# Kernel tuning notes

Hardware: AMD Instinct MI355X
Metric: run time of the kernel (lower is better)

The kernel has to match this reference:

```python
import jax, jax.numpy as jnp
import numpy as np

N_NODES = 500000
D = 128          # input_dim
UNITS = 128
K = 32           # neigh_max
B = 20000        # batch of target nodes
LEAKY_ALPHA = 0.2  # tf.nn.leaky_relu default


def setup_inputs() -> dict:
    key = jax.random.key(0)
    k1, k2, k3, k4, k5, k6, k7 = jax.random.split(key, 7)
    features = jax.random.normal(k1, (N_NODES, D), dtype=jnp.float32)
    node = jax.random.randint(k2, (B, 1), 0, N_NODES, dtype=jnp.int32)
    neighbours = jax.random.randint(k3, (B, K), 0, N_NODES, dtype=jnp.int32)
    # learned parameters (glorot-scale random)
    kernel = jax.random.normal(k4, (1, D, D), dtype=jnp.float32) * (1.0 / np.sqrt(D))
    kernel1 = jax.random.normal(k5, (1, D, D), dtype=jnp.float32) * (1.0 / np.sqrt(D))
    attention_weights = jax.random.normal(k6, (1, 2 * D), dtype=jnp.float32) * (1.0 / np.sqrt(2 * D))
    neigh_weights = jax.random.normal(k7, (D, UNITS), dtype=jnp.float32) * (1.0 / np.sqrt(D))
    return {
        "features": features,
        "node": node,
        "neighbours": neighbours,
        "kernel": kernel,
        "kernel1": kernel1,
        "attention_weights": attention_weights,
        "neigh_weights": neigh_weights,
    }


def reference(features, node, neighbours, kernel, kernel1, attention_weights, neigh_weights):
    # gather: node_feat [B,1,D], neigh_feat [B,K,D]
    node_feat = features[node]
    neigh_feat = features[neighbours]
    # per-node projections (kernel tiled over batch in original == shared matmul)
    node_h = jnp.einsum('bkd,de->bke', node_feat, kernel[0])    # [B,1,D]
    neigh_h = jnp.einsum('bkd,de->bke', neigh_feat, kernel1[0])  # [B,K,D]
    # concat [neigh, tiled node] -> [B,K,2D]
    tile_node = jnp.broadcast_to(node_h, neigh_h.shape)
    concat_feat = jnp.concatenate([neigh_h, tile_node], axis=2)
    # attention score: [B,K,2D] @ [2D,1] -> [B,K,1], leaky_relu (alpha=0.2)
    score = concat_feat @ attention_weights.reshape(2 * D, 1)
    score = jnp.where(score > 0, score, LEAKY_ALPHA * score)
    # softmax over neighbors (axis K)
    final_score = jax.nn.softmax(score, axis=1)                  # [B,K,1]
    # weighted aggregate: neigh_h^T @ score -> [B,D]
    attention_feat = jnp.einsum('bkd,bk->bd', neigh_h, final_score[..., 0])
    # output projection
    return attention_feat @ neigh_weights                        # [B,UNITS]
```

## Files before the change

kernel.cpp:

```cpp
#include <hip/hip_runtime.h>
#include <hip/hip_bf16.h>

#define D 128
#define K 32
#define NB 20000
#define NPB 4
#define NBLK (NB / NPB)
#define NROWS 33
#define RSTRIDE 66

typedef unsigned short u16;
typedef unsigned int   u32;

__device__ inline float blo(u32 v) { return __uint_as_float(v << 16); }
__device__ inline float bhi(u32 v) { return __uint_as_float(v & 0xffff0000u); }
__device__ inline u32 f2b_rne(float x) {
    u32 u = __float_as_uint(x);
    return (u + 0x7fffu + ((u >> 16) & 1u)) >> 16;
}
__device__ inline u32 pack2(float a, float b) { return f2b_rne(a) | (f2b_rne(b) << 16); }

__global__ __launch_bounds__(256)
void precompute_kernel(const float* __restrict__ k0, const float* __restrict__ k1,
                       const float* __restrict__ aw, const float* __restrict__ nw,
                       float* __restrict__ w12, u16* __restrict__ MTb)
{
    int t = threadIdx.x;
    if (blockIdx.x < 64) {
        int gid = blockIdx.x * 256 + t;
        int u = gid & 127, d = gid >> 7;
        float acc = 0.f;
        #pragma unroll 8
        for (int e = 0; e < D; ++e)
            acc = fmaf(k1[d * D + e], nw[e * D + u], acc);
        MTb[u * D + d] = (u16)f2b_rne(acc);
    } else {
        if (t < 128) {
            float acc = 0.f;
            #pragma unroll 8
            for (int e = 0; e < D; ++e)
                acc = fmaf(k1[t * D + e], aw[e], acc);
            w12[t] = acc;
        } else {
            int d = t - 128;
            float acc = 0.f;
            #pragma unroll 8
            for (int e = 0; e < D; ++e)
                acc = fmaf(k0[d * D + e], aw[128 + e], acc);
            w12[t] = acc;
        }
    }
}

__global__ __launch_bounds__(256)
void gat4_kernel(const float* __restrict__ features,
                 const int* __restrict__ node,
                 const int* __restrict__ neigh,
                 const float* __restrict__ w12g,
                 const u16* __restrict__ MTb,
                 float* __restrict__ out)
{
    __shared__ u32   fbuf[132 * RSTRIDE];
    __shared__ float wlds[256];
    __shared__ int   idxs[132];
    __shared__ float zb[132];
    __shared__ float alpha[128];
    __shared__ float agg[512];

    const int t  = threadIdx.x;
    const int b4 = blockIdx.x * NPB;

    wlds[t] = w12g[t];
    if (t < 132) {
        int n = t & 3, j = t >> 2;
        idxs[t] = (j < K) ? neigh[(b4 + n) * K + j] : node[b4 + n];
    }
    __syncthreads();

    const float4* f4 = (const float4*)features;
    #pragma unroll 4
    for (int c = t; c < 132 * 32; c += 256) {
        int r = c >> 5, cc = c & 31;
        float4 v = f4[(size_t)idxs[r] * 32 + cc];
        u32* dst = &fbuf[r * RSTRIDE + cc * 2];
        dst[0] = pack2(v.x, v.y);
        dst[1] = pack2(v.z, v.w);
        const float* w = &wlds[((r < 128) ? 0 : 128) + cc * 4];
        float p = v.x * w[0] + v.y * w[1] + v.z * w[2] + v.w * w[3];
        p += __shfl_xor(p, 1);
        p += __shfl_xor(p, 2);
        p += __shfl_xor(p, 4);
        p += __shfl_xor(p, 8);
        p += __shfl_xor(p, 16);
        if (cc == 0) zb[(r & 3) * 33 + (r >> 2)] = p;
    }
    __syncthreads();

    if ((t & 63) == 0) {
        int n = t >> 6;
        float cadd = zb[n * 33 + 32];
        float m = -1e30f;
        #pragma unroll
        for (int k = 0; k < K; ++k) {
            float v = zb[n * 33 + k] + cadd;
            v = v > 0.f ? v : 0.2f * v;
            alpha[n * 32 + k] = v;
            m = fmaxf(m, v);
        }
        float s = 0.f;
        #pragma unroll
        for (int k = 0; k < K; ++k) {
            float e = __expf(alpha[n * 32 + k] - m);
            alpha[n * 32 + k] = e;
            s += e;
        }
        float inv = 1.f / s;
        #pragma unroll
        for (int k = 0; k < K; ++k) alpha[n * 32 + k] *= inv;
    }
    __syncthreads();

    {
        int n = t >> 6, p = t & 63;
        float a0 = 0.f, a1 = 0.f;
        #pragma unroll
        for (int k = 0; k < K; ++k) {
            u32 v = fbuf[(4 * k + n) * RSTRIDE + p];
            float al = alpha[n * 32 + k];
            a0 = fmaf(al, blo(v), a0);
            a1 = fmaf(al, bhi(v), a1);
        }
        agg[n * 128 + 2 * p]     = a0;
        agg[n * 128 + 2 * p + 1] = a1;
    }
    __syncthreads();

    {
        int u  = t & 127;
        int nA = t >> 7;
        const uint4* mrow = (const uint4*)(MTb + u * D);
        const float* aggA = &agg[nA * 128];
        const float* aggB = &agg[(nA + 2) * 128];
        float accA0 = 0.f, accA1 = 0.f, accB0 = 0.f, accB1 = 0.f;
        #pragma unroll
        for (int q = 0; q < 16; ++q) {
            uint4 m4 = mrow[q];
            int d0 = q * 8;
            float m0 = blo(m4.x), m1 = bhi(m4.x), m2 = blo(m4.y), m3 = bhi(m4.y);
            float m4f = blo(m4.z), m5 = bhi(m4.z), m6 = blo(m4.w), m7 = bhi(m4.w);
            accA0 += aggA[d0] * m0 + aggA[d0+1] * m1 + aggA[d0+2] * m2 + aggA[d0+3] * m3;
            accA1 += aggA[d0+4] * m4f + aggA[d0+5] * m5 + aggA[d0+6] * m6 + aggA[d0+7] * m7;
            accB0 += aggB[d0] * m0 + aggB[d0+1] * m1 + aggB[d0+2] * m2 + aggB[d0+3] * m3;
            accB1 += aggB[d0+4] * m4f + aggB[d0+5] * m5 + aggB[d0+6] * m6 + aggB[d0+7] * m7;
        }
        out[(size_t)(b4 + nA) * D + u]     = accA0 + accA1;
        out[(size_t)(b4 + nA + 2) * D + u] = accB0 + accB1;
    }
}

#define RS 33
#define RSF 132
__global__ __launch_bounds__(256)
void gat_fallback_kernel(const float* __restrict__ features, const int* __restrict__ node,
                         const int* __restrict__ neigh,
                         const float* __restrict__ k0, const float* __restrict__ k1,
                         const float* __restrict__ aw, const float* __restrict__ nw,
                         float* __restrict__ out)
{
    __shared__ float4 fbuf[NROWS * RS];
    __shared__ float w1[D], w2[D], h[D];
    __shared__ int   idxs[NROWS];
    __shared__ float psum[NROWS][8];
    __shared__ float zb[NROWS], alpha[K], agg[D];

    const int b = blockIdx.x, t = threadIdx.x;

    if (t < 128) {
        float a = 0.f;
        for (int e = 0; e < D; ++e) a = fmaf(k1[t * D + e], aw[e], a);
        w1[t] = a;
    } else {
        int d = t - 128;
        float a = 0.f;
        for (int e = 0; e < D; ++e) a = fmaf(k0[d * D + e], aw[128 + e], a);
        w2[d] = a;
    }
    if (t < K)       idxs[t] = neigh[b * K + t];
    else if (t == K) idxs[K] = node[b];
    __syncthreads();

    const float4* f4 = (const float4*)features;
    for (int c = t; c < NROWS * 32; c += 256) {
        int j = c >> 5, cc = c & 31;
        fbuf[j * RS + cc] = f4[(size_t)idxs[j] * 32 + cc];
    }
    __syncthreads();

    for (int task = t; task < NROWS * 8; task += 256) {
        int j = task >> 3, sub = task & 7;
        const float* w = (j < K) ? w1 : w2;
        const float4* r = &fbuf[j * RS + sub * 4];
        int d0 = sub * 16;
        float4 a0 = r[0], a1 = r[1], a2 = r[2], a3 = r[3];
        float acc;
        acc  = a0.x * w[d0 + 0]  + a0.y * w[d0 + 1]  + a0.z * w[d0 + 2]  + a0.w * w[d0 + 3];
        acc += a1.x * w[d0 + 4]  + a1.y * w[d0 + 5]  + a1.z * w[d0 + 6]  + a1.w * w[d0 + 7];
        acc += a2.x * w[d0 + 8]  + a2.y * w[d0 + 9]  + a2.z * w[d0 + 10] + a2.w * w[d0 + 11];
        acc += a3.x * w[d0 + 12] + a3.y * w[d0 + 13] + a3.z * w[d0 + 14] + a3.w * w[d0 + 15];
        psum[j][sub] = acc;
    }
    __syncthreads();

    if (t < NROWS) {
        float s = 0.f;
        #pragma unroll
        for (int i = 0; i < 8; ++i) s += psum[t][i];
        zb[t] = s;
    }
    __syncthreads();

    if (t == 0) {
        float c = zb[K];
        float m = -1e30f;
        #pragma unroll
        for (int k = 0; k < K; ++k) {
            float v = zb[k] + c;
            v = v > 0.f ? v : 0.2f * v;
            zb[k] = v;
            m = fmaxf(m, v);
        }
        float s = 0.f;
        #pragma unroll
        for (int k = 0; k < K; ++k) { float e = __expf(zb[k] - m); alpha[k] = e; s += e; }
        float inv = 1.f / s;
        #pragma unroll
        for (int k = 0; k < K; ++k) alpha[k] *= inv;
    }
    __syncthreads();

    const float* fb = (const float*)fbuf;
    if (t < D) {
        float a = 0.f;
        #pragma unroll
        for (int k = 0; k < K; ++k)
            a = fmaf(alpha[k], fb[k * RSF + t], a);
        agg[t] = a;
    }
    __syncthreads();

    if (t < 128) {
        float acc = 0.f;
        for (int d = 0; d < D; ++d) acc = fmaf(agg[d], k1[d * D + t], acc);
        h[t] = acc;
    }
    __syncthreads();
    if (t < 128) {
        float acc = 0.f;
        for (int e = 0; e < D; ++e) acc = fmaf(h[e], nw[e * D + t], acc);
        out[(size_t)b * D + t] = acc;
    }
}

extern "C" void kernel_launch(void* const* d_in, const int* in_sizes, int n_in,
                              void* d_out, int out_size, void* d_ws, size_t ws_size,
                              hipStream_t stream) {
    const float* features = (const float*)d_in[0];
    const int*   node     = (const int*)d_in[1];
    const int*   neigh    = (const int*)d_in[2];
    const float* k0       = (const float*)d_in[3];
    const float* k1       = (const float*)d_in[4];
    const float* aw       = (const float*)d_in[5];
    const float* nw       = (const float*)d_in[6];

    const size_t need = 256 * sizeof(float) + (size_t)D * D * sizeof(u16);
    if (ws_size >= need) {
        float* w12 = (float*)d_ws;
        u16*   MTb = (u16*)(w12 + 256);
        precompute_kernel<<<65, 256, 0, stream>>>(k0, k1, aw, nw, w12, MTb);
        gat4_kernel<<<NBLK, 256, 0, stream>>>(features, node, neigh, w12, MTb,
                                              (float*)d_out);
    } else {
        gat_fallback_kernel<<<NB, 256, 0, stream>>>(features, node, neigh,
                                                    k0, k1, aw, nw, (float*)d_out);
    }
}
```

Before: 412.1 us.

## Batch all gather loads in registers and do softmax with wave shuffles

Each thread now loads its 17 neighbour and node indices straight into registers and issues all 17 float4 feature gathers before any use. This drops the index staging through LDS and its barrier and raises memory-level parallelism. The softmax moves from a single thread per node to a 32-lane shuffle reduction, and the attention weights are broadcast with __shfl, which removes the alpha LDS array and one barrier. The change costs more registers, which may lower occupancy, and drops the padded row stride, which may bring LDS bank conflicts.

```diff
diff --git a/kernel.cpp b/kernel.cpp
--- a/kernel.cpp
+++ b/kernel.cpp
@@ -7,7 +7,7 @@
 #define NPB 4
 #define NBLK (NB / NPB)
 #define NROWS 33
-#define RSTRIDE 66
+#define FSTR 64
 
 typedef unsigned short u16;
 typedef unsigned int   u32;
@@ -60,33 +60,40 @@
                  const u16* __restrict__ MTb,
                  float* __restrict__ out)
 {
-    __shared__ u32   fbuf[132 * RSTRIDE];
-    __shared__ float wlds[256];
-    __shared__ int   idxs[132];
+    __shared__ u32   fbuf[128 * FSTR];
     __shared__ float zb[132];
-    __shared__ float alpha[128];
     __shared__ float agg[512];
 
     const int t  = threadIdx.x;
     const int b4 = blockIdx.x * NPB;
-
-    wlds[t] = w12g[t];
-    if (t < 132) {
-        int n = t & 3, j = t >> 2;
-        idxs[t] = (j < K) ? neigh[(b4 + n) * K + j] : node[b4 + n];
-    }
-    __syncthreads();
+    const int cc = t & 31;
+    const int r0 = t >> 5;
+
+    const float4* w4 = (const float4*)w12g;
+    const float4 wlo = w4[cc];
+    const float4 whi = w4[32 + cc];
+
+    int idx[17];
+    #pragma unroll
+    for (int i = 0; i < 16; ++i) {
+        int r = r0 + 8 * i;
+        idx[i] = neigh[(b4 + (r & 3)) * K + (r >> 2)];
+    }
+    idx[16] = node[b4 + (r0 & 3)];
 
     const float4* f4 = (const float4*)features;
-    #pragma unroll 4
-    for (int c = t; c < 132 * 32; c += 256) {
-        int r = c >> 5, cc = c & 31;
-        float4 v = f4[(size_t)idxs[r] * 32 + cc];
-        u32* dst = &fbuf[r * RSTRIDE + cc * 2];
-        dst[0] = pack2(v.x, v.y);
-        dst[1] = pack2(v.z, v.w);
-        const float* w = &wlds[((r < 128) ? 0 : 128) + cc * 4];
-        float p = v.x * w[0] + v.y * w[1] + v.z * w[2] + v.w * w[3];
+    float4 v[17];
+    #pragma unroll
+    for (int i = 0; i < 17; ++i)
+        v[i] = f4[(size_t)idx[i] * 32 + cc];
+
+    #pragma unroll
+    for (int i = 0; i < 16; ++i) {
+        int r = r0 + 8 * i;
+        u32* dst = &fbuf[r * FSTR + cc * 2];
+        dst[0] = pack2(v[i].x, v[i].y);
+        dst[1] = pack2(v[i].z, v[i].w);
+        float p = v[i].x * wlo.x + v[i].y * wlo.y + v[i].z * wlo.z + v[i].w * wlo.w;
         p += __shfl_xor(p, 1);
         p += __shfl_xor(p, 2);
         p += __shfl_xor(p, 4);
@@ -94,44 +101,46 @@
         p += __shfl_xor(p, 16);
         if (cc == 0) zb[(r & 3) * 33 + (r >> 2)] = p;
     }
-    __syncthreads();
-
-    if ((t & 63) == 0) {
-        int n = t >> 6;
-        float cadd = zb[n * 33 + 32];
-        float m = -1e30f;
+    if (r0 < 4) {
+        float p = v[16].x * whi.x + v[16].y * whi.y + v[16].z * whi.z + v[16].w * whi.w;
+        p += __shfl_xor(p, 1);
+        p += __shfl_xor(p, 2);
+        p += __shfl_xor(p, 4);
+        p += __shfl_xor(p, 8);
+        p += __shfl_xor(p, 16);
+        if (cc == 0) zb[r0 * 33 + 32] = p;
+    }
+    __syncthreads();
+
+    {
+        const int n = t >> 6, l = t & 63, k32 = l & 31;
+        float vsc = zb[n * 33 + k32] + zb[n * 33 + 32];
+        vsc = vsc > 0.f ? vsc : 0.2f * vsc;
+        float m = vsc;
+        m = fmaxf(m, __shfl_xor(m, 1));
+        m = fmaxf(m, __shfl_xor(m, 2));
+        m = fmaxf(m, __shfl_xor(m, 4));
+        m = fmaxf(m, __shfl_xor(m, 8));
+        m = fmaxf(m, __shfl_xor(m, 16));
+        float e = __expf(vsc - m);
+        float s = e;
+        s += __shfl_xor(s, 1);
+        s += __shfl_xor(s, 2);
+        s += __shfl_xor(s, 4);
+        s += __shfl_xor(s, 8);
+        s += __shfl_xor(s, 16);
+        const float a = e * (1.0f / s);
+
+        float a0 = 0.f, a1 = 0.f;
         #pragma unroll
         for (int k = 0; k < K; ++k) {
-            float v = zb[n * 33 + k] + cadd;
-            v = v > 0.f ? v : 0.2f * v;
-            alpha[n * 32 + k] = v;
-            m = fmaxf(m, v);
-        }
-        float s = 0.f;
-        #pragma unroll
-        for (int k = 0; k < K; ++k) {
-            float e = __expf(alpha[n * 32 + k] - m);
-            alpha[n * 32 + k] = e;
-            s += e;
-        }
-        float inv = 1.f / s;
-        #pragma unroll
-        for (int k = 0; k < K; ++k) alpha[n * 32 + k] *= inv;
-    }
-    __syncthreads();
-
-    {
-        int n = t >> 6, p = t & 63;
-        float a0 = 0.f, a1 = 0.f;
-        #pragma unroll
-        for (int k = 0; k < K; ++k) {
-            u32 v = fbuf[(4 * k + n) * RSTRIDE + p];
-            float al = alpha[n * 32 + k];
-            a0 = fmaf(al, blo(v), a0);
-            a1 = fmaf(al, bhi(v), a1);
-        }
-        agg[n * 128 + 2 * p]     = a0;
-        agg[n * 128 + 2 * p + 1] = a1;
+            float al = __shfl(a, k);
+            u32 vv = fbuf[(4 * k + n) * FSTR + l];
+            a0 = fmaf(al, blo(vv), a0);
+            a1 = fmaf(al, bhi(vv), a1);
+        }
+        agg[n * 128 + 2 * l]     = a0;
+        agg[n * 128 + 2 * l + 1] = a1;
     }
     __syncthreads();
 
```

Result: faster. 385.2 us (-6.5%).
